# Performance work log

Measured on AMD Instinct MI355X. Metric: run time of the kernel, lower is better.

## Reference

```python
import jax, jax.numpy as jnp
import numpy as np

B, S, D = 16, 256, 256      # batch, seq_len, input_size (= 2*hidden)
H = 128                     # hidden size per direction
NL = 2                      # num layers
A = 8                       # n_actions
DK = D // 4                 # attention projection dim = 64
SRU_IN = 2 * D              # cat(rnn_input, attn_pool) = 512


def setup_inputs() -> dict:
    key = jax.random.key(0)
    ks = jax.random.split(key, 12)
    stdv = 1.0 / np.sqrt(DK)
    inp = {
        "x": jax.random.normal(ks[0], (B, S, D), jnp.float32),
        "x_mask": jnp.zeros((B, S), bool),
        "actions": jax.random.randint(ks[1], (B,), 0, A),
        # SeqAttentionAction params (reset_parameters: uniform(-stdv,stdv), biases zero)
        "w1": jax.random.uniform(ks[2], (A, D, DK), jnp.float32, -stdv, stdv),
        "b1": jnp.zeros((A, DK), jnp.float32),
        "w2": jax.random.uniform(ks[3], (A, D, DK), jnp.float32, -stdv, stdv),
        "b2": jnp.zeros((A, DK), jnp.float32),
        "v": jax.random.uniform(ks[4], (A, DK), jnp.float32, -stdv, stdv),
        # SRU params: per layer, forward & backward cells. k=4 slices (x~, f, r, highway)
        "sru_w_f": jax.random.uniform(ks[5], (NL, SRU_IN, 4 * H), jnp.float32, -0.05, 0.05),
        "sru_b_f": jnp.zeros((NL, 2 * H), jnp.float32),
        "sru_w_b": jax.random.uniform(ks[6], (NL, SRU_IN, 4 * H), jnp.float32, -0.05, 0.05),
        "sru_b_b": jnp.zeros((NL, 2 * H), jnp.float32),
    }
    return inp


def _sru_layer(X, W, b):
    """SRU (use_tanh=1). X:(S,B,Din) -> (S,B,H)."""
    U = jnp.einsum("sbd,dk->sbk", X, W)           # (S,B,4H)
    u0, uf, ur, hw = jnp.split(U, 4, axis=-1)
    bf, br = jnp.split(b, 2)
    f = jax.nn.sigmoid(uf + bf)
    r = jax.nn.sigmoid(ur + br)

    def step(c, t):
        f_t, u_t, r_t, hw_t = t
        c = f_t * c + (1.0 - f_t) * u_t
        h = r_t * jnp.tanh(c) + (1.0 - r_t) * hw_t
        return c, h

    c0 = jnp.zeros((X.shape[1], f.shape[-1]), X.dtype)
    _, hs = jax.lax.scan(step, c0, (f, u0, r, hw))
    return hs


def _attn_pools(memory, rnn_input, x_mask, w1a, b1a, w2a, b2a, va):
    """Action-conditioned tanh attention, vectorized over all timesteps.
    memory:(B,L,D) rnn_input:(S,B,D) -> pools:(S,B,D) (detached, as in torch .data)."""
    xt = jnp.einsum("bld,bdk->blk", memory, w1a) + b1a[:, None]    # (B,L,K)
    yt = jnp.einsum("sbd,bdk->sbk", rnn_input, w2a) + b2a[None]    # (S,B,K)
    t = jnp.tanh(xt[None] + yt[:, :, None])                        # (S,B,L,K)
    scores = jnp.einsum("sblk,bk->sbl", t, va)                     # (S,B,L)
    scores = jnp.where(x_mask[None], -jnp.inf, scores)
    att = jax.nn.softmax(scores, axis=-1)
    pools = jnp.einsum("sbl,bld->sbd", att, memory)
    return jax.lax.stop_gradient(pools)


def reference(x, x_mask, actions, w1, b1, w2, b2, v,
              sru_w_f, sru_b_f, sru_w_b, sru_b_b):
    memory = x                                # (B,L,D)
    out = jnp.transpose(x, (1, 0, 2))         # (S,B,D)
    # one-hot matmul selection == gather by action index
    w1a, b1a = w1[actions], b1[actions]
    w2a, b2a = w2[actions], b2[actions]
    va = v[actions]
    for i in range(NL):
        pools = _attn_pools(memory, out, x_mask, w1a, b1a, w2a, b2a, va)
        inputs = jnp.concatenate([out, pools], axis=2)   # (S,B,2D); inputs_f == inputs_b
        hf = _sru_layer(inputs, sru_w_f[i], sru_b_f[i])
        hb = _sru_layer(inputs, sru_w_b[i], sru_b_b[i])
        out = jnp.concatenate([hf, hb], axis=2)          # (S,B,2H)=(S,B,D)
    return jnp.transpose(out, (1, 0, 2))                 # (B,S,D)
```

## Files before the change

### kernel.cpp

```cpp
#include <hip/hip_runtime.h>
#include <hip/hip_bf16.h>

#define S_ 256
#define D_ 256
#define K_ 64
#define SIN 512
#define F4H 512

typedef unsigned short u16;
typedef __attribute__((ext_vector_type(8))) short short8;
typedef __attribute__((ext_vector_type(4))) float f32x4;

__device__ __forceinline__ float rcpf(float x) { return __builtin_amdgcn_rcpf(x); }
__device__ __forceinline__ float fast_sigmoid(float x) {
  return rcpf(1.0f + __expf(-x));
}
__device__ __forceinline__ float fast_tanh(float x) {
  return 1.0f - 2.0f * rcpf(__expf(2.0f * x) + 1.0f);
}
__device__ __forceinline__ u16 f2bf(float f) {
  unsigned int u = __float_as_uint(f);
  return (u16)((u + 0x7fff + ((u >> 16) & 1)) >> 16);
}

__global__ __launch_bounds__(256) void k_prep(const float* __restrict__ sw_f,
    const float* __restrict__ sw_b, u16* __restrict__ wt,
    const float* __restrict__ x, u16* __restrict__ xT,
    const int* __restrict__ araw, int* __restrict__ act_out,
    int* __restrict__ status) {
  if (blockIdx.x == 0 && blockIdx.y == 0 && blockIdx.z == 0 && threadIdx.x == 0) {
    bool oddzero = true;
    for (int i = 1; i < 16; i += 2) oddzero = oddzero && (araw[i] == 0);
    bool ok = true;
    for (int b = 0; b < 16; ++b) {
      int v = oddzero ? araw[2 * b] : araw[b];
      act_out[b] = (v < 0) ? 0 : (v > 7 ? 7 : v);
      ok = ok && (v >= 0 && v < 8);
    }
    *status = ok ? 1 : 0;
  }
  __shared__ u16 tile[64][66];
  int tj = threadIdx.x & 63, ti = threadIdx.x >> 6;
  int z = blockIdx.z;
  if (z < 4) {
    int layer = z >> 1;
    const float* src = (z & 1) ? sw_b : sw_f;
    int k0 = blockIdx.x * 64, n0 = blockIdx.y * 64;
#pragma unroll
    for (int i = ti; i < 64; i += 4)
      tile[i][tj] = f2bf(src[layer * 262144 + (k0 + i) * 512 + n0 + tj]);
    __syncthreads();
#pragma unroll
    for (int j = ti; j < 64; j += 4)
      wt[z * 262144 + (n0 + j) * 512 + k0 + tj] = tile[tj][j];
  } else {
    if (blockIdx.x >= 4 || blockIdx.y >= 4) return;
    int b = z - 4;
    int l0 = blockIdx.x * 64, d0 = blockIdx.y * 64;
#pragma unroll
    for (int i = ti; i < 64; i += 4)
      tile[i][tj] = f2bf(x[b * 65536 + (l0 + i) * 256 + d0 + tj]);
    __syncthreads();
#pragma unroll
    for (int j = ti; j < 64; j += 4)
      xT[b * 65536 + (d0 + j) * 256 + l0 + tj] = tile[tj][j];
  }
}

__global__ __launch_bounds__(256) void k_xt(const float* __restrict__ x,
    const int* __restrict__ act, const float* __restrict__ w1,
    const float* __restrict__ b1, float* __restrict__ xtT) {
  __shared__ float As[16][17], Bs[16][68];
  int b = blockIdx.y;
  int a = act[b];
  int l0 = blockIdx.x * 16;
  const float* A = x + b * (S_ * D_);
  const float* W = w1 + a * (D_ * K_);
  int tid = threadIdx.x;
  int ty = tid >> 4, tx = tid & 15;
  float acc[4] = {};
  for (int kk = 0; kk < D_; kk += 16) {
    As[ty][tx] = A[(l0 + ty) * D_ + kk + tx];
    *(float4*)&Bs[ty][tx << 2] = *(const float4*)(W + (kk + ty) * K_ + (tx << 2));
    __syncthreads();
#pragma unroll
    for (int k = 0; k < 16; ++k) {
      float av = As[ty][k];
      acc[0] += av * Bs[k][(tx << 2) + 0];
      acc[1] += av * Bs[k][(tx << 2) + 1];
      acc[2] += av * Bs[k][(tx << 2) + 2];
      acc[3] += av * Bs[k][(tx << 2) + 3];
    }
    __syncthreads();
  }
#pragma unroll
  for (int j = 0; j < 4; ++j) {
    int n = (tx << 2) + j;
    xtT[(b << 14) + n * 256 + l0 + ty] = acc[j] + b1[a * K_ + n];
  }
}

__global__ __launch_bounds__(256) void k_yt(const float* __restrict__ curb,
    int sstride, int bstride, const int* __restrict__ act,
    const float* __restrict__ w2, const float* __restrict__ b2,
    float* __restrict__ yt) {
  __shared__ float As[16][17], Bs[16][68];
  int b = blockIdx.y;
  int a = act[b];
  int s0 = blockIdx.x * 16;
  const float* A = curb + b * bstride;
  const float* W = w2 + a * (D_ * K_);
  int tid = threadIdx.x;
  int ty = tid >> 4, tx = tid & 15;
  float acc[4] = {};
  for (int kk = 0; kk < D_; kk += 16) {
    As[ty][tx] = A[(s0 + ty) * sstride + kk + tx];
    *(float4*)&Bs[ty][tx << 2] = *(const float4*)(W + (kk + ty) * K_ + (tx << 2));
    __syncthreads();
#pragma unroll
    for (int k = 0; k < 16; ++k) {
      float av = As[ty][k];
      acc[0] += av * Bs[k][(tx << 2) + 0];
      acc[1] += av * Bs[k][(tx << 2) + 1];
      acc[2] += av * Bs[k][(tx << 2) + 2];
      acc[3] += av * Bs[k][(tx << 2) + 3];
    }
    __syncthreads();
  }
  float4 o;
  o.x = acc[0] + b2[a * K_ + (tx << 2) + 0];
  o.y = acc[1] + b2[a * K_ + (tx << 2) + 1];
  o.z = acc[2] + b2[a * K_ + (tx << 2) + 2];
  o.w = acc[3] + b2[a * K_ + (tx << 2) + 3];
  *(float4*)(yt + ((s0 + ty) * 16 + b) * K_ + (tx << 2)) = o;
}

__global__ __launch_bounds__(256) void k_score(const float* __restrict__ xtT,
    const float* __restrict__ yt, const float* __restrict__ v,
    const int* __restrict__ act, const unsigned char* __restrict__ xmask,
    u16* __restrict__ scores) {
  __shared__ float yts[4][K_], vas[K_];
  __shared__ float redm[4][4], reds[4][4];
  int tid = threadIdx.x;
  int bid = blockIdx.x;
  int b = bid & 15, s4 = bid >> 4;
  int a = act[b];
  if (tid < 64) vas[tid] = v[a * K_ + tid];
  {
    int row = tid >> 6, k = tid & 63;
    yts[row][k] = yt[((s4 * 4 + row) * 16 + b) * K_ + k];
  }
  __syncthreads();
  float acc0 = 0.f, acc1 = 0.f, acc2 = 0.f, acc3 = 0.f;
  {
    const float* xb = xtT + (b << 14) + tid;
#pragma unroll
    for (int k = 0; k < 64; ++k) {
      float xv = xb[k * 256];
      float vv = vas[k];
      acc0 += vv * fast_tanh(xv + yts[0][k]);
      acc1 += vv * fast_tanh(xv + yts[1][k]);
      acc2 += vv * fast_tanh(xv + yts[2][k]);
      acc3 += vv * fast_tanh(xv + yts[3][k]);
    }
    if (xmask[b * S_ + tid]) { acc0 = acc1 = acc2 = acc3 = -1e30f; }
  }
  int wid = tid >> 6;
  float m0 = acc0, m1 = acc1, m2 = acc2, m3 = acc3;
#pragma unroll
  for (int d = 32; d; d >>= 1) {
    m0 = fmaxf(m0, __shfl_xor(m0, d));
    m1 = fmaxf(m1, __shfl_xor(m1, d));
    m2 = fmaxf(m2, __shfl_xor(m2, d));
    m3 = fmaxf(m3, __shfl_xor(m3, d));
  }
  if ((tid & 63) == 0) {
    redm[0][wid] = m0; redm[1][wid] = m1; redm[2][wid] = m2; redm[3][wid] = m3;
  }
  __syncthreads();
  m0 = fmaxf(fmaxf(redm[0][0], redm[0][1]), fmaxf(redm[0][2], redm[0][3]));
  m1 = fmaxf(fmaxf(redm[1][0], redm[1][1]), fmaxf(redm[1][2], redm[1][3]));
  m2 = fmaxf(fmaxf(redm[2][0], redm[2][1]), fmaxf(redm[2][2], redm[2][3]));
  m3 = fmaxf(fmaxf(redm[3][0], redm[3][1]), fmaxf(redm[3][2], redm[3][3]));
  float p0 = __expf(acc0 - m0), p1 = __expf(acc1 - m1);
  float p2 = __expf(acc2 - m2), p3 = __expf(acc3 - m3);
  float s0 = p0, s1 = p1, s2 = p2, s3 = p3;
#pragma unroll
  for (int d = 32; d; d >>= 1) {
    s0 += __shfl_xor(s0, d);
    s1 += __shfl_xor(s1, d);
    s2 += __shfl_xor(s2, d);
    s3 += __shfl_xor(s3, d);
  }
  if ((tid & 63) == 0) {
    reds[0][wid] = s0; reds[1][wid] = s1; reds[2][wid] = s2; reds[3][wid] = s3;
  }
  __syncthreads();
  s0 = reds[0][0] + reds[0][1] + reds[0][2] + reds[0][3];
  s1 = reds[1][0] + reds[1][1] + reds[1][2] + reds[1][3];
  s2 = reds[2][0] + reds[2][1] + reds[2][2] + reds[2][3];
  s3 = reds[3][0] + reds[3][1] + reds[3][2] + reds[3][3];
  u16* dst = scores + ((s4 * 4) * 16 + b) * 256 + tid;
  dst[0]        = f2bf(p0 * rcpf(s0));
  dst[16 * 256] = f2bf(p1 * rcpf(s1));
  dst[32 * 256] = f2bf(p2 * rcpf(s2));
  dst[48 * 256] = f2bf(p3 * rcpf(s3));
}

__global__ __launch_bounds__(256) void k_poolm(const u16* __restrict__ scores,
    const u16* __restrict__ xT, const float* __restrict__ curb,
    int sstride, int bstride, u16* __restrict__ inp) {
  __shared__ u16 As[64][72];
  __shared__ u16 Bs[64][72];
  int b = blockIdx.z;
  int m0 = blockIdx.x * 64, n0 = blockIdx.y * 64;
  int tid = threadIdx.x;
  int wid = tid >> 6, lane = tid & 63;
  int wm = wid >> 1, wn = wid & 1;
  f32x4 acc[2][2];
#pragma unroll
  for (int i = 0; i < 2; ++i)
#pragma unroll
    for (int j = 0; j < 2; ++j) acc[i][j] = (f32x4){0.f, 0.f, 0.f, 0.f};
  int srow = tid >> 2, soff = (tid & 3) * 16;
  int lrow = lane & 15, lk = (lane >> 4) << 3;
  for (int kk = 0; kk < 256; kk += 64) {
    const u16* ga = scores + ((m0 + srow) * 16 + b) * 256 + kk + soff;
    const u16* gb = xT + b * 65536 + (n0 + srow) * 256 + kk + soff;
    *(short8*)&As[srow][soff]     = *(const short8*)(ga);
    *(short8*)&As[srow][soff + 8] = *(const short8*)(ga + 8);
    *(short8*)&Bs[srow][soff]     = *(const short8*)(gb);
    *(short8*)&Bs[srow][soff + 8] = *(const short8*)(gb + 8);
    __syncthreads();
#pragma unroll
    for (int ks = 0; ks < 2; ++ks) {
      short8 af[2], bf[2];
#pragma unroll
      for (int mi = 0; mi < 2; ++mi)
        af[mi] = *(const short8*)&As[wm * 32 + mi * 16 + lrow][ks * 32 + lk];
#pragma unroll
      for (int ni = 0; ni < 2; ++ni)
        bf[ni] = *(const short8*)&Bs[wn * 32 + ni * 16 + lrow][ks * 32 + lk];
#pragma unroll
      for (int mi = 0; mi < 2; ++mi)
#pragma unroll
        for (int ni = 0; ni < 2; ++ni)
          acc[mi][ni] = __builtin_amdgcn_mfma_f32_16x16x32_bf16(
              af[mi], bf[ni], acc[mi][ni], 0, 0, 0);
    }
    __syncthreads();
  }
#pragma unroll
  for (int mi = 0; mi < 2; ++mi)
#pragma unroll
    for (int ni = 0; ni < 2; ++ni) {
      int r0 = m0 + wm * 32 + mi * 16 + ((lane >> 4) << 2);
      int c = n0 + wn * 32 + ni * 16 + (lane & 15);
#pragma unroll
      for (int r = 0; r < 4; ++r)
        inp[((r0 + r) * 16 + b) * SIN + 256 + c] = f2bf(acc[mi][ni][r]);
    }
#pragma unroll
  for (int i = 0; i < 4; ++i) {
    int idx = i * 256 + tid;
    int so = idx >> 4, d4 = (idx & 15) << 2;
    float4 v4 = *(const float4*)(curb + b * bstride + (m0 + so) * sstride + n0 + d4);
    ushort4 o;
    o.x = f2bf(v4.x); o.y = f2bf(v4.y); o.z = f2bf(v4.z); o.w = f2bf(v4.w);
    *(ushort4*)(inp + ((m0 + so) * 16 + b) * SIN + n0 + d4) = o;
  }
}

__global__ __launch_bounds__(256) void k_mfma(const u16* __restrict__ inp,
    const u16* __restrict__ wt, float* __restrict__ Uf, float* __restrict__ Ub,
    int layer) {
  __shared__ u16 As[128][72];
  __shared__ u16 Bs[64][72];
  float* U = blockIdx.z ? Ub : Uf;
  const u16* W = wt + (layer * 2 + blockIdx.z) * 262144;
  int m0 = blockIdx.x * 128, n0 = blockIdx.y * 64;
  int tid = threadIdx.x;
  int wid = tid >> 6, lane = tid & 63;
  int wm = wid >> 1, wn = wid & 1;
  f32x4 acc[4][2];
#pragma unroll
  for (int i = 0; i < 4; ++i)
#pragma unroll
    for (int j = 0; j < 2; ++j) acc[i][j] = (f32x4){0.f, 0.f, 0.f, 0.f};
  int arow = tid >> 1, ahalf = tid & 1;
  int brow = tid >> 2, bq = tid & 3;
  int lrow = lane & 15, lk = (lane >> 4) << 3;
  for (int kk = 0; kk < 512; kk += 64) {
    const u16* ga = inp + (m0 + arow) * SIN + kk + ahalf * 32;
    const u16* gb = W + (n0 + brow) * 512 + kk + bq * 16;
#pragma unroll
    for (int j = 0; j < 4; ++j)
      *(short8*)&As[arow][ahalf * 32 + j * 8] = *(const short8*)(ga + j * 8);
    *(short8*)&Bs[brow][bq * 16]     = *(const short8*)(gb);
    *(short8*)&Bs[brow][bq * 16 + 8] = *(const short8*)(gb + 8);
    __syncthreads();
#pragma unroll
    for (int ks = 0; ks < 2; ++ks) {
      short8 af[4], bf[2];
#pragma unroll
      for (int mi = 0; mi < 4; ++mi)
        af[mi] = *(const short8*)&As[wm * 64 + mi * 16 + lrow][ks * 32 + lk];
#pragma unroll
      for (int ni = 0; ni < 2; ++ni)
        bf[ni] = *(const short8*)&Bs[wn * 32 + ni * 16 + lrow][ks * 32 + lk];
#pragma unroll
      for (int mi = 0; mi < 4; ++mi)
#pragma unroll
        for (int ni = 0; ni < 2; ++ni)
          acc[mi][ni] = __builtin_amdgcn_mfma_f32_16x16x32_bf16(
              af[mi], bf[ni], acc[mi][ni], 0, 0, 0);
    }
    __syncthreads();
  }
#pragma unroll
  for (int mi = 0; mi < 4; ++mi)
#pragma unroll
    for (int ni = 0; ni < 2; ++ni) {
      int r0 = m0 + wm * 64 + mi * 16 + ((lane >> 4) << 2);
      int c = n0 + wn * 32 + ni * 16 + (lane & 15);
#pragma unroll
      for (int r = 0; r < 4; ++r)
        U[(r0 + r) * F4H + c] = acc[mi][ni][r];
    }
}

__global__ __launch_bounds__(256) void k_scan(const float* __restrict__ Uf,
    const float* __restrict__ Ub, const float* __restrict__ bfp,
    const float* __restrict__ bbp, float* __restrict__ obase,
    int o_sstride, int o_bstride, const int* __restrict__ status, int final) {
  __shared__ float so[16][257];
  __shared__ float sA[16][17], sB[16][17], sC[16][17];
  int tid = threadIdx.x;
  int c16 = tid & 15;
  int seg = tid >> 4;
  int chain = blockIdx.x * 16 + c16;
  int dir = chain >> 11;
  int rem = chain & 2047;
  int b = rem >> 7, h = rem & 127;
  const float* U = dir ? Ub : Uf;
  const float* bias = dir ? bbp : bfp;
  float bfv = bias[h], brv = bias[128 + h];
  const float* up = U + b * 512 + h;
  int s0 = seg * 16;
  float fv[16], u0[16], rv[16], hw[16];
#pragma unroll
  for (int t = 0; t < 16; ++t) {
    const float* q = up + (s0 + t) * 8192;
    u0[t] = q[0]; fv[t] = q[128]; rv[t] = q[256]; hw[t] = q[384];
  }
  float A = 1.f, Bv = 0.f;
#pragma unroll
  for (int t = 0; t < 16; ++t) {
    float f = fast_sigmoid(fv[t] + bfv);
    fv[t] = f;
    Bv = f * Bv + (1.f - f) * u0[t];
    A = A * f;
  }
  sA[seg][c16] = A;
  sB[seg][c16] = Bv;
  __syncthreads();
  if (tid < 16) {
    float prevB = 0.f;
#pragma unroll
    for (int sgi = 0; sgi < 16; ++sgi) {
      sC[sgi][tid] = prevB;
      prevB = sA[sgi][tid] * prevB + sB[sgi][tid];
    }
  }
  __syncthreads();
  float c = sC[seg][c16];
#pragma unroll
  for (int t = 0; t < 16; ++t) {
    float f = fv[t];
    c = f * (c - u0[t]) + u0[t];
    float r = fast_sigmoid(rv[t] + brv);
    so[c16][s0 + t] = r * fast_tanh(c) + (1.f - r) * hw[t];
  }
  __syncthreads();
  bool ok = final ? (*status != 0) : true;
  int h_idx = tid & 15, s_idx = tid >> 4;
  int c2 = blockIdx.x * 16 + h_idx;
  int dir2 = c2 >> 11, rem2 = c2 & 2047;
  int b2 = rem2 >> 7, h2 = rem2 & 127;
  float* op2 = obase + b2 * o_bstride + dir2 * 128 + h2;
#pragma unroll
  for (int j = 0; j < 16; ++j) {
    int s = s_idx * 16 + j;
    float hv = so[h_idx][s];
    op2[s * o_sstride] = ok ? hv : 20.0f;
  }
}

__global__ __launch_bounds__(256) void k_fill(float* out, float v, int n) {
  int idx = blockIdx.x * 256 + threadIdx.x;
  if (idx < n) out[idx] = v;
}

extern "C" void kernel_launch(void* const* d_in, const int* in_sizes, int n_in,
                              void* d_out, int out_size, void* d_ws, size_t ws_size,
                              hipStream_t stream) {
  float* out = (float*)d_out;
  int fill_grid = (out_size + 255) / 256;

  const int exp_sizes[12] = {1048576, 4096, 16, 131072, 512, 131072, 512, 512,
                             524288, 512, 524288, 512};
  bool env_ok = (n_in == 12);
  if (env_ok)
    for (int i = 0; i < 12; ++i) env_ok = env_ok && (in_sizes[i] == exp_sizes[i]);
  if (!env_ok) {
    k_fill<<<fill_grid, 256, 0, stream>>>(out, 10.0f, out_size);
    return;
  }

  const float* x    = (const float*)d_in[0];
  const unsigned char* xmask = (const unsigned char*)d_in[1];
  const float* w1   = (const float*)d_in[3];
  const float* b1   = (const float*)d_in[4];
  const float* w2   = (const float*)d_in[5];
  const float* b2   = (const float*)d_in[6];
  const float* v    = (const float*)d_in[7];
  const float* sw_f = (const float*)d_in[8];
  const float* sb_f = (const float*)d_in[9];
  const float* sw_b = (const float*)d_in[10];
  const float* sb_b = (const float*)d_in[11];

  float* ws = (float*)d_ws;
  size_t off = 0;
  float* pb0    = ws + off; off += 1048576;
  float* xtT    = ws + off; off += 262144;
  float* yt     = ws + off; off += 262144;
  float* Uf     = ws + off; off += 2097152;
  float* Ub     = ws + off; off += 2097152;
  u16*   scores = (u16*)(ws + off); off += 524288;
  u16*   xT     = (u16*)(ws + off); off += 524288;
  u16*   inp    = (u16*)(ws + off); off += 1048576;
  u16*   wt     = (u16*)(ws + off); off += 524288;
  int*   act    = (int*)(ws + off); off += 16;
  int*   status = (int*)(ws + off); off += 16;

  if (ws_size < off * sizeof(float)) {
    k_fill<<<fill_grid, 256, 0, stream>>>(out, 30.0f, out_size);
    return;
  }

  k_prep<<<dim3(8, 8, 20), 256, 0, stream>>>(sw_f, sw_b, wt, x, xT,
      (const int*)d_in[2], act, status);
  k_xt<<<dim3(16, 16), 256, 0, stream>>>(x, act, w1, b1, xtT);

  for (int layer = 0; layer < 2; ++layer) {
    const float* curb = layer ? pb0 : x;
    int sstride = layer ? 4096 : 256;
    int bstride = layer ? 256 : 65536;
    float* nxt      = layer ? out : pb0;
    int o_sstride   = layer ? 256 : 4096;
    int o_bstride   = layer ? 65536 : 256;
    k_yt<<<dim3(16, 16), 256, 0, stream>>>(curb, sstride, bstride, act, w2, b2, yt);
    k_score<<<1024, 256, 0, stream>>>(xtT, yt, v, act, xmask, scores);
    k_poolm<<<dim3(4, 4, 16), 256, 0, stream>>>(scores, xT, curb, sstride,
                                                bstride, inp);
    k_mfma<<<dim3(32, 8, 2), 256, 0, stream>>>(inp, wt, Uf, Ub, layer);
    k_scan<<<256, 256, 0, stream>>>(Uf, Ub, sb_f + layer * 256, sb_b + layer * 256,
                                    nxt, o_sstride, o_bstride, status, layer);
  }
}
```

Before: 142.9 us.

## Store SRU gate projections in bf16 and score 8 query rows per block

The SRU projection output U is now written as bf16 instead of fp32 and widened back in the scan kernel, halving the write and read traffic of the largest intermediate buffers. Separately, the attention score kernel processes 8 query rows per block instead of 4, so each loaded xt value is reused across twice as many tanh evaluations, and it launches half as many blocks. The bf16 storage of the gate pre-activations adds rounding error in the recurrence, and the wider score blocks raise register pressure while giving fewer blocks to spread across the GPU.

```diff
diff --git a/kernel.cpp b/kernel.cpp
--- a/kernel.cpp
+++ b/kernel.cpp
@@ -21,6 +21,9 @@
 __device__ __forceinline__ u16 f2bf(float f) {
   unsigned int u = __float_as_uint(f);
   return (u16)((u + 0x7fff + ((u >> 16) & 1)) >> 16);
+}
+__device__ __forceinline__ float bf2f(u16 u) {
+  return __uint_as_float(((unsigned int)u) << 16);
 }
 
 __global__ __launch_bounds__(256) void k_prep(const float* __restrict__ sw_f,
@@ -139,72 +142,70 @@
     const float* __restrict__ yt, const float* __restrict__ v,
     const int* __restrict__ act, const unsigned char* __restrict__ xmask,
     u16* __restrict__ scores) {
-  __shared__ float yts[4][K_], vas[K_];
-  __shared__ float redm[4][4], reds[4][4];
+  __shared__ float yts[8][K_], vas[K_];
+  __shared__ float redm[8][4], reds[8][4];
   int tid = threadIdx.x;
   int bid = blockIdx.x;
-  int b = bid & 15, s4 = bid >> 4;
+  int b = bid & 15, s8 = bid >> 4;
   int a = act[b];
   if (tid < 64) vas[tid] = v[a * K_ + tid];
-  {
-    int row = tid >> 6, k = tid & 63;
-    yts[row][k] = yt[((s4 * 4 + row) * 16 + b) * K_ + k];
-  }
-  __syncthreads();
-  float acc0 = 0.f, acc1 = 0.f, acc2 = 0.f, acc3 = 0.f;
+#pragma unroll
+  for (int i = tid; i < 512; i += 256) {
+    int row = i >> 6, k = i & 63;
+    yts[row][k] = yt[((s8 * 8 + row) * 16 + b) * K_ + k];
+  }
+  __syncthreads();
+  float acc[8] = {};
   {
     const float* xb = xtT + (b << 14) + tid;
 #pragma unroll
     for (int k = 0; k < 64; ++k) {
       float xv = xb[k * 256];
       float vv = vas[k];
-      acc0 += vv * fast_tanh(xv + yts[0][k]);
-      acc1 += vv * fast_tanh(xv + yts[1][k]);
-      acc2 += vv * fast_tanh(xv + yts[2][k]);
-      acc3 += vv * fast_tanh(xv + yts[3][k]);
-    }
-    if (xmask[b * S_ + tid]) { acc0 = acc1 = acc2 = acc3 = -1e30f; }
+#pragma unroll
+      for (int r = 0; r < 8; ++r)
+        acc[r] += vv * fast_tanh(xv + yts[r][k]);
+    }
+    if (xmask[b * S_ + tid]) {
+#pragma unroll
+      for (int r = 0; r < 8; ++r) acc[r] = -1e30f;
+    }
   }
   int wid = tid >> 6;
-  float m0 = acc0, m1 = acc1, m2 = acc2, m3 = acc3;
-#pragma unroll
-  for (int d = 32; d; d >>= 1) {
-    m0 = fmaxf(m0, __shfl_xor(m0, d));
-    m1 = fmaxf(m1, __shfl_xor(m1, d));
-    m2 = fmaxf(m2, __shfl_xor(m2, d));
-    m3 = fmaxf(m3, __shfl_xor(m3, d));
-  }
+  float m[8];
+#pragma unroll
+  for (int r = 0; r < 8; ++r) m[r] = acc[r];
+#pragma unroll
+  for (int d = 32; d; d >>= 1)
+#pragma unroll
+    for (int r = 0; r < 8; ++r) m[r] = fmaxf(m[r], __shfl_xor(m[r], d));
   if ((tid & 63) == 0) {
-    redm[0][wid] = m0; redm[1][wid] = m1; redm[2][wid] = m2; redm[3][wid] = m3;
-  }
-  __syncthreads();
-  m0 = fmaxf(fmaxf(redm[0][0], redm[0][1]), fmaxf(redm[0][2], redm[0][3]));
-  m1 = fmaxf(fmaxf(redm[1][0], redm[1][1]), fmaxf(redm[1][2], redm[1][3]));
-  m2 = fmaxf(fmaxf(redm[2][0], redm[2][1]), fmaxf(redm[2][2], redm[2][3]));
-  m3 = fmaxf(fmaxf(redm[3][0], redm[3][1]), fmaxf(redm[3][2], redm[3][3]));
-  float p0 = __expf(acc0 - m0), p1 = __expf(acc1 - m1);
-  float p2 = __expf(acc2 - m2), p3 = __expf(acc3 - m3);
-  float s0 = p0, s1 = p1, s2 = p2, s3 = p3;
-#pragma unroll
-  for (int d = 32; d; d >>= 1) {
-    s0 += __shfl_xor(s0, d);
-    s1 += __shfl_xor(s1, d);
-    s2 += __shfl_xor(s2, d);
-    s3 += __shfl_xor(s3, d);
-  }
+#pragma unroll
+    for (int r = 0; r < 8; ++r) redm[r][wid] = m[r];
+  }
+  __syncthreads();
+#pragma unroll
+  for (int r = 0; r < 8; ++r)
+    m[r] = fmaxf(fmaxf(redm[r][0], redm[r][1]), fmaxf(redm[r][2], redm[r][3]));
+  float p[8], s[8];
+#pragma unroll
+  for (int r = 0; r < 8; ++r) { p[r] = __expf(acc[r] - m[r]); s[r] = p[r]; }
+#pragma unroll
+  for (int d = 32; d; d >>= 1)
+#pragma unroll
+    for (int r = 0; r < 8; ++r) s[r] += __shfl_xor(s[r], d);
   if ((tid & 63) == 0) {
-    reds[0][wid] = s0; reds[1][wid] = s1; reds[2][wid] = s2; reds[3][wid] = s3;
-  }
-  __syncthreads();
-  s0 = reds[0][0] + reds[0][1] + reds[0][2] + reds[0][3];
-  s1 = reds[1][0] + reds[1][1] + reds[1][2] + reds[1][3];
-  s2 = reds[2][0] + reds[2][1] + reds[2][2] + reds[2][3];
-  s3 = reds[3][0] + reds[3][1] + reds[3][2] + reds[3][3];
-  u16* dst = scores + ((s4 * 4) * 16 + b) * 256 + tid;
-  dst[0]        = f2bf(p0 * rcpf(s0));
-  dst[16 * 256] = f2bf(p1 * rcpf(s1));
-  dst[32 * 256] = f2bf(p2 * rcpf(s2));
-  dst[48 * 256] = f2bf(p3 * rcpf(s3));
+#pragma unroll
+    for (int r = 0; r < 8; ++r) reds[r][wid] = s[r];
+  }
+  __syncthreads();
+#pragma unroll
+  for (int r = 0; r < 8; ++r)
+    s[r] = reds[r][0] + reds[r][1] + reds[r][2] + reds[r][3];
+  u16* dst = scores + ((s8 * 8) * 16 + b) * 256 + tid;
+#pragma unroll
+  for (int r = 0; r < 8; ++r)
+    dst[r * 16 * 256] = f2bf(p[r] * rcpf(s[r]));
 }
 
 __global__ __launch_bounds__(256) void k_poolm(const u16* __restrict__ scores,
@@ -272,11 +273,11 @@
 }
 
 __global__ __launch_bounds__(256) void k_mfma(const u16* __restrict__ inp,
-    const u16* __restrict__ wt, float* __restrict__ Uf, float* __restrict__ Ub,
+    const u16* __restrict__ wt, u16* __restrict__ Uf, u16* __restrict__ Ub,
     int layer) {
   __shared__ u16 As[128][72];
   __shared__ u16 Bs[64][72];
-  float* U = blockIdx.z ? Ub : Uf;
+  u16* U = blockIdx.z ? Ub : Uf;
   const u16* W = wt + (layer * 2 + blockIdx.z) * 262144;
   int m0 = blockIdx.x * 128, n0 = blockIdx.y * 64;
   int tid = threadIdx.x;
@@ -325,12 +326,12 @@
       int c = n0 + wn * 32 + ni * 16 + (lane & 15);
 #pragma unroll
       for (int r = 0; r < 4; ++r)
-        U[(r0 + r) * F4H + c] = acc[mi][ni][r];
-    }
-}
-
-__global__ __launch_bounds__(256) void k_scan(const float* __restrict__ Uf,
-    const float* __restrict__ Ub, const float* __restrict__ bfp,
+        U[(r0 + r) * F4H + c] = f2bf(acc[mi][ni][r]);
+    }
+}
+
+__global__ __launch_bounds__(256) void k_scan(const u16* __restrict__ Uf,
+    const u16* __restrict__ Ub, const float* __restrict__ bfp,
     const float* __restrict__ bbp, float* __restrict__ obase,
     int o_sstride, int o_bstride, const int* __restrict__ status, int final) {
   __shared__ float so[16][257];
@@ -342,16 +343,17 @@
   int dir = chain >> 11;
   int rem = chain & 2047;
   int b = rem >> 7, h = rem & 127;
-  const float* U = dir ? Ub : Uf;
+  const u16* U = dir ? Ub : Uf;
   const float* bias = dir ? bbp : bfp;
   float bfv = bias[h], brv = bias[128 + h];
-  const float* up = U + b * 512 + h;
+  const u16* up = U + b * 512 + h;
   int s0 = seg * 16;
   float fv[16], u0[16], rv[16], hw[16];
 #pragma unroll
   for (int t = 0; t < 16; ++t) {
-    const float* q = up + (s0 + t) * 8192;
-    u0[t] = q[0]; fv[t] = q[128]; rv[t] = q[256]; hw[t] = q[384];
+    const u16* q = up + (s0 + t) * 8192;
+    u0[t] = bf2f(q[0]); fv[t] = bf2f(q[128]);
+    rv[t] = bf2f(q[256]); hw[t] = bf2f(q[384]);
   }
   float A = 1.f, Bv = 0.f;
 #pragma unroll
@@ -434,8 +436,8 @@
   float* pb0    = ws + off; off += 1048576;
   float* xtT    = ws + off; off += 262144;
   float* yt     = ws + off; off += 262144;
-  float* Uf     = ws + off; off += 2097152;
-  float* Ub     = ws + off; off += 2097152;
+  u16*   Uf     = (u16*)(ws + off); off += 1048576;
+  u16*   Ub     = (u16*)(ws + off); off += 1048576;
   u16*   scores = (u16*)(ws + off); off += 524288;
   u16*   xT     = (u16*)(ws + off); off += 524288;
   u16*   inp    = (u16*)(ws + off); off += 1048576;
@@ -460,7 +462,7 @@
     int o_sstride   = layer ? 256 : 4096;
     int o_bstride   = layer ? 65536 : 256;
     k_yt<<<dim3(16, 16), 256, 0, stream>>>(curb, sstride, bstride, act, w2, b2, yt);
-    k_score<<<1024, 256, 0, stream>>>(xtT, yt, v, act, xmask, scores);
+    k_score<<<512, 256, 0, stream>>>(xtT, yt, v, act, xmask, scores);
     k_poolm<<<dim3(4, 4, 16), 256, 0, stream>>>(scores, xT, curb, sstride,
                                                 bstride, inp);
     k_mfma<<<dim3(32, 8, 2), 256, 0, stream>>>(inp, wt, Uf, Ub, layer);
```

New measurement: 152.8 us. +6.9%, slower.
